# Performance work log

Hardware: AMD Instinct MI355X
Metric: run time of the kernel (lower is better)

The kernel has to match this reference:

```python
import jax, jax.numpy as jnp
import numpy as np

B, T, IN_DIM, D, H, NC = 4, 1024, 231, 512, 8, 1296
NL = 8          # 4 encoders x 2 layers each
DFF = 4 * D     # 2048
DH = D // H
EPS = 1e-5


def _p(k, shape, scale=0.02):
    return jax.random.normal(k, shape, jnp.float32) * scale


def setup_inputs() -> dict:
    key = jax.random.key(0)
    ks = iter(jax.random.split(key, 32))
    z = jnp.zeros
    o = jnp.ones
    return {
        'poses': jax.random.normal(next(ks), (B, T, IN_DIM), jnp.float32),
        'embed_w': _p(next(ks), (D, IN_DIM)), 'embed_b': z((D,)),
        'ln0_g': o((D,)), 'ln0_b': z((D,)),
        'inw': _p(next(ks), (NL, 3 * D, D)), 'inb': z((NL, 3 * D)),
        'outw': _p(next(ks), (NL, D, D)), 'outb': z((NL, D)),
        'ln1g': o((NL, D)), 'ln1b': z((NL, D)),
        'ln2g': o((NL, D)), 'ln2b': z((NL, D)),
        'ff1w': _p(next(ks), (NL, DFF, D)), 'ff1b': z((NL, DFF)),
        'ff2w': _p(next(ks), (NL, D, DFF)), 'ff2b': z((NL, D)),
        'conv1w': _p(next(ks), (D, D, 5)), 'conv1b': z((D,)),
        'bn1g': o((D,)), 'bn1b': z((D,)), 'bn1m': z((D,)), 'bn1v': o((D,)),
        'conv2w': _p(next(ks), (D, D, 3)), 'conv2b': z((D,)),
        'bn2g': o((D,)), 'bn2b': z((D,)), 'bn2m': z((D,)), 'bn2v': o((D,)),
        'fc1w': _p(next(ks), (D // 2, D)), 'fc1b': z((D // 2,)),
        'fc2w': _p(next(ks), (NC, D // 2)), 'fc2b': z((NC,)),
    }


def _ln(x, g, b):
    m = x.mean(-1, keepdims=True)
    v = x.var(-1, keepdims=True)
    return (x - m) / jnp.sqrt(v + EPS) * g + b


def _pos_enc(t_len, d, dtype):
    inv_freq = 1.0 / (10000.0 ** (jnp.arange(0, d, 2, dtype=jnp.float32) / d))
    sin_inp = jnp.arange(t_len, dtype=jnp.float32)[:, None] * inv_freq[None, :]  # [T, d/2]
    # interleave: even idx -> sin, odd idx -> cos
    return jnp.stack([jnp.sin(sin_inp), jnp.cos(sin_inp)], -1).reshape(t_len, d).astype(dtype)


def _layer(x, inw, inb, outw, outb, ln1g, ln1b, ln2g, ln2b, ff1w, ff1b, ff2w, ff2b):
    # pre-norm-style custom layer: norm1 before attention, residual add (no final norm)
    b_, t_, d_ = x.shape
    h = _ln(x, ln1g, ln1b)
    qkv = h @ inw.T + inb
    q, k, v = jnp.split(qkv, 3, axis=-1)
    heads = lambda z: z.reshape(b_, t_, H, DH).transpose(0, 2, 1, 3)  # [B,H,T,dh]
    q, k, v = heads(q), heads(k), heads(v)
    scores = jnp.einsum('bhqd,bhkd->bhqk', q, k) / np.float32(np.sqrt(DH))
    a = jax.nn.softmax(scores, axis=-1)  # explicit weights, as in torch need_weights=True path
    ctx = jnp.einsum('bhqk,bhkd->bhqd', a, v).transpose(0, 2, 1, 3).reshape(b_, t_, d_)
    x = x + ctx @ outw.T + outb
    h2 = _ln(x, ln2g, ln2b)
    ff = jax.nn.relu(h2 @ ff1w.T + ff1b) @ ff2w.T + ff2b
    return x + ff


def _bn(x, g, b, m, v):  # eval-mode BatchNorm1d over [B,C,T]
    return (x - m[None, :, None]) / jnp.sqrt(v + EPS)[None, :, None] * g[None, :, None] + b[None, :, None]


def _conv1d(x, w, b, pad):
    y = jax.lax.conv_general_dilated(x, w, (1,), ((pad, pad),),
                                     dimension_numbers=('NCH', 'OIH', 'NCH'))
    return y + b[None, :, None]


def reference(poses, embed_w, embed_b, ln0_g, ln0_b, inw, inb, outw, outb,
              ln1g, ln1b, ln2g, ln2b, ff1w, ff1b, ff2w, ff2b,
              conv1w, conv1b, bn1g, bn1b, bn1m, bn1v,
              conv2w, conv2b, bn2g, bn2b, bn2m, bn2v,
              fc1w, fc1b, fc2w, fc2b):
    x = _ln(poses @ embed_w.T + embed_b, ln0_g, ln0_b)
    x = x + _pos_enc(x.shape[1], D, x.dtype)[None]

    def block(y, idx):
        for i in idx:
            y = _layer(y, inw[i], inb[i], outw[i], outb[i], ln1g[i], ln1b[i],
                       ln2g[i], ln2b[i], ff1w[i], ff1b[i], ff2w[i], ff2b[i])
        return y

    x = block(x, (0, 1))
    x = block(x, (2, 3)) + x
    x = block(x, (4, 5)) + x
    x = block(x, (6, 7)) + x

    x = x.transpose(0, 2, 1)  # [B, D, T]
    tc = x.shape[-1]
    x = x.reshape(x.shape[0], x.shape[1], tc // 2, 2).mean(-1)  # AvgPool1d(2,2)
    x = jax.nn.gelu(_bn(_conv1d(x, conv1w, conv1b, 2), bn1g, bn1b, bn1m, bn1v), approximate=False)
    x = jax.nn.gelu(_bn(_conv1d(x, conv2w, conv2b, 1), bn2g, bn2b, bn2m, bn2v), approximate=False)
    x = x.transpose(0, 2, 1)  # [B, T/2, D]
    h = jax.nn.gelu(x @ fc1w.T + fc1b, approximate=False)
    return h @ fc2w.T + fc2b  # [B, T/2, num_classes]
```

## Files before the change

### kernel.cpp

```cpp
#include <hip/hip_runtime.h>
#include <math.h>

using u16 = unsigned short;
typedef __attribute__((ext_vector_type(8))) __bf16 bf16x8;
typedef __attribute__((ext_vector_type(4))) float f32x4;

constexpr int Bn = 4, Tn = 1024, INDIM = 231, Dm = 512, NCn = 1296;
constexpr int T2 = 512;
constexpr int Mseq = Bn * Tn;
constexpr int Mtc  = Bn * T2;

enum { EPI_BIAS = 0, EPI_BIAS_RELU, EPI_BIAS_RES, EPI_BIAS_GELU, EPI_SS_GELU };

__device__ __forceinline__ float gelu_exact(float x) {
    return 0.5f * x * (1.0f + erff(x * 0.70710678118654752f));
}
__device__ __forceinline__ u16 f2b(float f) {
    unsigned u = __builtin_bit_cast(unsigned, f);
    return (u16)((u + 0x7FFFu + ((u >> 16) & 1u)) >> 16);
}
__device__ __forceinline__ unsigned pack2(float a, float b) {
    return (unsigned)f2b(a) | ((unsigned)f2b(b) << 16);
}

typedef __attribute__((address_space(3))) void lds_void;
typedef __attribute__((address_space(1))) void g_void;
__device__ __forceinline__ void gld16(const void* g, void* l) {
    __builtin_amdgcn_global_load_lds((g_void*)(uintptr_t)g, (lds_void*)(uintptr_t)l, 16, 0, 0);
}

template<int EPI, bool OB, int IPAD, int OPAD, int MT>
__global__ __launch_bounds__(256)
void gemm_bf(const u16* __restrict__ A, int lda,
             const u16* __restrict__ W,
             float* __restrict__ Cf, u16* __restrict__ Cb,
             int M, int N, int K,
             const float* __restrict__ bias, const float* __restrict__ resid,
             const float* __restrict__ scale, const float* __restrict__ shift)
{
    constexpr int NR = (MT == 128) ? 4 : 2;
    constexpr int AI = MT / 32;
    __shared__ __align__(16) u16 As[2][MT * 64];
    __shared__ __align__(16) u16 Bs[2][128 * 64];
    const int tid = threadIdx.x;
    const int bm = blockIdx.y * MT, bn = blockIdx.x * 128;
    const int w = tid >> 6, lane = tid & 63;
    const int wr = (MT == 128) ? (w >> 1) * 64 : 0;
    const int wc = (MT == 128) ? (w & 1) * 64 : w * 32;
    const int lr = lane & 15, lhi = lane >> 4;

    const int srow = tid >> 3;
    const int cg8 = ((tid & 7) ^ (srow & 7)) * 8;
    const u16* apg[AI];
#pragma unroll
    for (int i = 0; i < AI; ++i) {
        const int r = bm + i * 32 + srow;
        apg[i] = A + (size_t)(r + 2 * IPAD * (r >> 9)) * lda + cg8;
    }
    const u16* wpg[4];
#pragma unroll
    for (int i = 0; i < 4; ++i) {
        int r = bn + i * 32 + srow; if (r >= N) r = N - 1;
        wpg[i] = W + (size_t)r * K + cg8;
    }

    f32x4 acc[4][NR] = {};
    const int nt = K >> 6;

#pragma unroll
    for (int i = 0; i < AI; ++i) gld16(apg[i], &As[0][(i * 256 + tid) * 8]);
#pragma unroll
    for (int i = 0; i < 4; ++i)  gld16(wpg[i], &Bs[0][(i * 256 + tid) * 8]);
    __syncthreads();

    for (int t = 0; t < nt; ++t) {
        const int cur = t & 1;
        if (t + 1 < nt) {
            const int k0 = (t + 1) * 64;
#pragma unroll
            for (int i = 0; i < AI; ++i) gld16(apg[i] + k0, &As[cur ^ 1][(i * 256 + tid) * 8]);
#pragma unroll
            for (int i = 0; i < 4; ++i)  gld16(wpg[i] + k0, &Bs[cur ^ 1][(i * 256 + tid) * 8]);
        }
#pragma unroll
        for (int ks = 0; ks < 2; ++ks) {
            bf16x8 af[4], bfv[NR];
#pragma unroll
            for (int m = 0; m < 4; ++m) {
                const int R = wr + lr + m * 16;
                af[m] = *(const bf16x8*)((const char*)&As[cur][0] + R * 128 + (((ks * 4 + lhi) ^ (R & 7)) * 16));
            }
#pragma unroll
            for (int n = 0; n < NR; ++n) {
                const int R = wc + lr + n * 16;
                bfv[n] = *(const bf16x8*)((const char*)&Bs[cur][0] + R * 128 + (((ks * 4 + lhi) ^ (R & 7)) * 16));
            }
#pragma unroll
            for (int m = 0; m < 4; ++m)
#pragma unroll
                for (int n = 0; n < NR; ++n)
                    acc[m][n] = __builtin_amdgcn_mfma_f32_16x16x32_bf16(af[m], bfv[n], acc[m][n], 0, 0, 0);
        }
        if (t + 1 < nt) __syncthreads();
    }

    const int col0 = bn + wc + lr;
    const int row0 = bm + wr + lhi * 4;
#pragma unroll
    for (int n = 0; n < NR; ++n) {
        const int col = col0 + n * 16;
        if (col >= N) continue;
        float bv = 0.f, sv = 0.f, hv = 0.f;
        if constexpr (EPI == EPI_SS_GELU) { sv = scale[col]; hv = shift[col]; }
        else bv = bias[col];
#pragma unroll
        for (int m = 0; m < 4; ++m) {
#pragma unroll
            for (int j = 0; j < 4; ++j) {
                const int r = row0 + m * 16 + j;
                const int orow = r + OPAD * (2 * (r >> 9) + 1);
                float o = acc[m][n][j];
                if constexpr (EPI == EPI_SS_GELU) {
                    o = gelu_exact(o * sv + hv);
                } else {
                    o += bv;
                    if constexpr (EPI == EPI_BIAS_RELU) o = fmaxf(o, 0.f);
                    if constexpr (EPI == EPI_BIAS_GELU) o = gelu_exact(o);
                    if constexpr (EPI == EPI_BIAS_RES) o += resid[(size_t)r * N + col];
                }
                if constexpr (OB) Cb[(size_t)orow * N + col] = f2b(o);
                else              Cf[(size_t)orow * N + col] = o;
            }
        }
    }
}

__global__ __launch_bounds__(256)
void attn_mfma(const u16* __restrict__ qkv, u16* __restrict__ out)
{
    const int b = blockIdx.z, h = blockIdx.y, q0 = blockIdx.x * 64;
    __shared__ __align__(16) u16 Ks[2][64 * 64];
    __shared__ __align__(16) u16 Vt[2][64 * 64];
    __shared__ __align__(16) float Ps[4][16 * 68];
    const int tid = threadIdx.x;
    const int w = tid >> 6, lane = tid & 63;
    const int lr = lane & 15, lhi = lane >> 4;
    const int kp = tid & 31, dc = (tid >> 5) * 8;
    const int krow = w * 8 + (lane >> 3);
    const int kcg = (((lane & 7) ^ (lane >> 3))) * 8;

    bf16x8 qf0, qf1;
    {
        const u16* qp = qkv + (size_t)(b * Tn + q0 + w * 16 + lr) * 1536 + h * 64 + lhi * 8;
        qf0 = *(const bf16x8*)qp;
        qf1 = *(const bf16x8*)(qp + 32);
    }
    float mrow[4], lrow[4];
#pragma unroll
    for (int j = 0; j < 4; ++j) { mrow[j] = -1e30f; lrow[j] = 0.f; }
    f32x4 oacc[4] = {};

    auto stageK = [&](int kb, int bsel) {
#pragma unroll
        for (int i = 0; i < 2; ++i)
            gld16(qkv + (size_t)(b * Tn + kb + i * 32 + krow) * 1536 + 512 + h * 64 + kcg,
                  &Ks[bsel][(i * 256 + tid) * 8]);
    };
    auto loadV = [&](int kb, uint4& rA, uint4& rB) {
        const u16* vp = qkv + (size_t)(b * Tn + kb + 2 * kp) * 1536 + 1024 + h * 64 + dc;
        rA = *(const uint4*)vp;
        rB = *(const uint4*)(vp + 1536);
    };
    auto vtrans = [&](uint4 rA, uint4 rB, int bsel) {
        const unsigned a0[4] = {rA.x, rA.y, rA.z, rA.w};
        const unsigned a1[4] = {rB.x, rB.y, rB.z, rB.w};
#pragma unroll
        for (int jj = 0; jj < 4; ++jj) {
            const int d0_ = dc + 2 * jj, d1_ = d0_ + 1;
            const unsigned w0 = (a0[jj] & 0xffffu) | (a1[jj] << 16);
            const unsigned w1 = (a0[jj] >> 16) | (a1[jj] & 0xffff0000u);
            *(unsigned*)((char*)&Vt[bsel][0] + d0_ * 128 + ((4 * kp) ^ ((d0_ & 7) << 4))) = w0;
            *(unsigned*)((char*)&Vt[bsel][0] + d1_ * 128 + ((4 * kp) ^ ((d1_ & 7) << 4))) = w1;
        }
    };

    uint4 vA, vB;
    stageK(0, 0);
    loadV(0, vA, vB);
    vtrans(vA, vB, 0);
    __syncthreads();

    constexpr float C1 = 0.125f * 1.44269504f;

    for (int kt = 0; kt < 16; ++kt) {
        const int cur = kt & 1;
        const bool more = kt < 15;
        if (more) {
            stageK((kt + 1) * 64, cur ^ 1);
            loadV((kt + 1) * 64, vA, vB);
        }
        __builtin_amdgcn_s_setprio(1);
        f32x4 s[4] = {};
#pragma unroll
        for (int t = 0; t < 4; ++t) {
            const int r = t * 16 + lr;
            const bf16x8 k0 = *(const bf16x8*)((const char*)&Ks[cur][0] + r * 128 + ((lhi * 16) ^ ((r & 7) << 4)));
            const bf16x8 k1 = *(const bf16x8*)((const char*)&Ks[cur][0] + r * 128 + ((64 + lhi * 16) ^ ((r & 7) << 4)));
            s[t] = __builtin_amdgcn_mfma_f32_16x16x32_bf16(qf0, k0, s[t], 0, 0, 0);
            s[t] = __builtin_amdgcn_mfma_f32_16x16x32_bf16(qf1, k1, s[t], 0, 0, 0);
        }
        __builtin_amdgcn_s_setprio(0);
        float f[4];
#pragma unroll
        for (int j = 0; j < 4; ++j) {
            float mt = fmaxf(fmaxf(s[0][j], s[1][j]), fmaxf(s[2][j], s[3][j]));
            mt = fmaxf(mt, __shfl_xor(mt, 1));
            mt = fmaxf(mt, __shfl_xor(mt, 2));
            mt = fmaxf(mt, __shfl_xor(mt, 4));
            mt = fmaxf(mt, __shfl_xor(mt, 8));
            const float mnew = fmaxf(mrow[j], mt);
            f[j] = exp2f((mrow[j] - mnew) * C1);
            mrow[j] = mnew;
            const float nb = mnew * C1;
            float sum = 0.f;
#pragma unroll
            for (int t = 0; t < 4; ++t) {
                const float p = exp2f(fmaf(s[t][j], C1, -nb));
                Ps[w][(lhi * 4 + j) * 68 + t * 16 + lr] = p;
                sum += p;
            }
            sum += __shfl_xor(sum, 1);
            sum += __shfl_xor(sum, 2);
            sum += __shfl_xor(sum, 4);
            sum += __shfl_xor(sum, 8);
            lrow[j] = lrow[j] * f[j] + sum;
        }
#pragma unroll
        for (int t = 0; t < 4; ++t)
#pragma unroll
            for (int j = 0; j < 4; ++j) oacc[t][j] *= f[j];
        asm volatile("s_waitcnt lgkmcnt(0)" ::: "memory");
        bf16x8 pf[2];
#pragma unroll
        for (int s2 = 0; s2 < 2; ++s2) {
            const float* pr = &Ps[w][lr * 68 + s2 * 32 + lhi * 8];
            const float4 pa = *(const float4*)pr;
            const float4 pb = *(const float4*)(pr + 4);
            uint4 pk;
            pk.x = pack2(pa.x, pa.y); pk.y = pack2(pa.z, pa.w);
            pk.z = pack2(pb.x, pb.y); pk.w = pack2(pb.z, pb.w);
            pf[s2] = __builtin_bit_cast(bf16x8, pk);
        }
        __builtin_amdgcn_s_setprio(1);
#pragma unroll
        for (int t = 0; t < 4; ++t) {
            const int rd = t * 16 + lr;
            const bf16x8 v0f = *(const bf16x8*)((const char*)&Vt[cur][0] + rd * 128 + ((lhi * 16) ^ ((rd & 7) << 4)));
            const bf16x8 v1f = *(const bf16x8*)((const char*)&Vt[cur][0] + rd * 128 + ((64 + lhi * 16) ^ ((rd & 7) << 4)));
            oacc[t] = __builtin_amdgcn_mfma_f32_16x16x32_bf16(pf[0], v0f, oacc[t], 0, 0, 0);
            oacc[t] = __builtin_amdgcn_mfma_f32_16x16x32_bf16(pf[1], v1f, oacc[t], 0, 0, 0);
        }
        __builtin_amdgcn_s_setprio(0);
        if (more) {
            vtrans(vA, vB, cur ^ 1);
            __syncthreads();
        }
    }
#pragma unroll
    for (int j = 0; j < 4; ++j) {
        const float inv = 1.f / lrow[j];
        const size_t grow = (size_t)(b * Tn + q0 + w * 16 + lhi * 4 + j) * 512 + h * 64;
#pragma unroll
        for (int t = 0; t < 4; ++t)
            out[grow + t * 16 + lr] = f2b(oacc[t][j] * inv);
    }
}

__device__ __forceinline__ float pe_val(int t, int d) {
    const int k = d & ~1;
    const float invf = __expf(-(float)k * (9.210340371976184f / 512.f));
    const float ang = (float)t * invf;
    return (d & 1) ? cosf(ang) : sinf(ang);
}

template<bool OB, bool PE>
__global__ __launch_bounds__(256)
void ln_k(const float* __restrict__ in, float* __restrict__ outf, u16* __restrict__ outb,
          const float* __restrict__ g, const float* __restrict__ bsh)
{
    const int lane = threadIdx.x & 63;
    const int row = blockIdx.x * 4 + (threadIdx.x >> 6);
    const float* src = in + (size_t)row * Dm;
    const int c0 = lane * 4;
    const float4 v0 = *(const float4*)(src + c0);
    const float4 v1 = *(const float4*)(src + 256 + c0);
    float s  = v0.x + v0.y + v0.z + v0.w + v1.x + v1.y + v1.z + v1.w;
    float ss = v0.x * v0.x + v0.y * v0.y + v0.z * v0.z + v0.w * v0.w
             + v1.x * v1.x + v1.y * v1.y + v1.z * v1.z + v1.w * v1.w;
#pragma unroll
    for (int off = 32; off; off >>= 1) { s += __shfl_xor(s, off); ss += __shfl_xor(ss, off); }
    const float mean = s * (1.f / 512.f);
    const float var = ss * (1.f / 512.f) - mean * mean;
    const float rstd = rsqrtf(var + 1e-5f);
    const float4 g0 = *(const float4*)(g + c0),   g1 = *(const float4*)(g + 256 + c0);
    const float4 b0 = *(const float4*)(bsh + c0), b1 = *(const float4*)(bsh + 256 + c0);
    float o0[4] = {(v0.x - mean) * rstd * g0.x + b0.x, (v0.y - mean) * rstd * g0.y + b0.y,
                   (v0.z - mean) * rstd * g0.z + b0.z, (v0.w - mean) * rstd * g0.w + b0.w};
    float o1[4] = {(v1.x - mean) * rstd * g1.x + b1.x, (v1.y - mean) * rstd * g1.y + b1.y,
                   (v1.z - mean) * rstd * g1.z + b1.z, (v1.w - mean) * rstd * g1.w + b1.w};
    if constexpr (PE) {
        const int t = row & (Tn - 1);
#pragma unroll
        for (int j = 0; j < 4; ++j) { o0[j] += pe_val(t, c0 + j); o1[j] += pe_val(t, 256 + c0 + j); }
    }
    if constexpr (OB) {
        *(ushort4*)(outb + (size_t)row * Dm + c0) =
            make_ushort4(f2b(o0[0]), f2b(o0[1]), f2b(o0[2]), f2b(o0[3]));
        *(ushort4*)(outb + (size_t)row * Dm + 256 + c0) =
            make_ushort4(f2b(o1[0]), f2b(o1[1]), f2b(o1[2]), f2b(o1[3]));
    } else {
        *(float4*)(outf + (size_t)row * Dm + c0) = make_float4(o0[0], o0[1], o0[2], o0[3]);
        *(float4*)(outf + (size_t)row * Dm + 256 + c0) = make_float4(o1[0], o1[1], o1[2], o1[3]);
    }
}

__global__ void copy_k(const float* __restrict__ a, float* __restrict__ o, int n4) {
    const int i = blockIdx.x * blockDim.x + threadIdx.x;
    if (i < n4) ((float4*)o)[i] = ((const float4*)a)[i];
}
__global__ void add_k(float* __restrict__ o, const float* __restrict__ a, int n4) {
    const int i = blockIdx.x * blockDim.x + threadIdx.x;
    if (i < n4) {
        float4 x = ((float4*)o)[i];
        const float4 y = ((const float4*)a)[i];
        x.x += y.x; x.y += y.y; x.z += y.z; x.w += y.w;
        ((float4*)o)[i] = x;
    }
}
__global__ void cvt_layer_k(const float* __restrict__ inw, const float* __restrict__ outw,
                            const float* __restrict__ ff1w, const float* __restrict__ ff2w,
                            int layer, u16* __restrict__ dst) {
    const int i = (blockIdx.x * 256 + threadIdx.x) * 8;
    const float* src;
    if (i < 786432)       src = inw  + (size_t)layer *  786432 + i;
    else if (i < 1048576) src = outw + (size_t)layer *  262144 + (i - 786432);
    else if (i < 2097152) src = ff1w + (size_t)layer * 1048576 + (i - 1048576);
    else                  src = ff2w + (size_t)layer * 1048576 + (i - 2097152);
    const float4 a = *(const float4*)src, b = *(const float4*)(src + 4);
    uint4 o; o.x = pack2(a.x, a.y); o.y = pack2(a.z, a.w); o.z = pack2(b.x, b.y); o.w = pack2(b.z, b.w);
    *(uint4*)(dst + i) = o;
}
__global__ void cvt8_k(const float* __restrict__ in, u16* __restrict__ out, int n8) {
    const int t = blockIdx.x * 256 + threadIdx.x;
    if (t >= n8) return;
    const int i = t * 8;
    const float4 a = *(const float4*)(in + i), b = *(const float4*)(in + i + 4);
    uint4 o; o.x = pack2(a.x, a.y); o.y = pack2(a.z, a.w); o.z = pack2(b.x, b.y); o.w = pack2(b.z, b.w);
    *(uint4*)(out + i) = o;
}
__global__ void padposes_k(const float* __restrict__ p, u16* __restrict__ o, int rows) {
    const int i = blockIdx.x * 256 + threadIdx.x;
    if (i >= rows * 256) return;
    const int r = i >> 8, c = i & 255;
    o[i] = (c < INDIM) ? f2b(p[r * INDIM + c]) : (u16)0;
}
__global__ void zero_k(uint4* __restrict__ p, int n16) {
    const int i = blockIdx.x * 256 + threadIdx.x;
    if (i < n16) p[i] = make_uint4(0, 0, 0, 0);
}
__global__ void pool_k(const float* __restrict__ x, u16* __restrict__ o) {
    const int i = blockIdx.x * 256 + threadIdx.x;
    if (i >= 262144) return;
    const int flat = i * 4;
    const int row = flat >> 9, col = flat & 511;
    const int b = row >> 9, t2 = row & 511;
    const float* p0 = x + ((size_t)(b * Tn + 2 * t2) << 9) + col;
    const float4 u = *(const float4*)p0;
    const float4 w = *(const float4*)(p0 + 512);
    ushort4 r = make_ushort4(f2b(0.5f * (u.x + w.x)), f2b(0.5f * (u.y + w.y)),
                             f2b(0.5f * (u.z + w.z)), f2b(0.5f * (u.w + w.w)));
    *(ushort4*)(o + (((size_t)(b * 516 + 2 + t2)) << 9) + col) = r;
}
__global__ void wtrans_k(const float* __restrict__ w, u16* __restrict__ wt, int KS) {
    const int i = blockIdx.x * 256 + threadIdx.x;
    if (i >= 512 * 512 * KS) return;
    const int o = i / (512 * KS);
    const int rem = i - o * (512 * KS);
    const int c = rem / KS, ks = rem - c * KS;
    wt[((size_t)o * KS + ks) * 512 + c] = f2b(w[i]);
}
__global__ void bnfold_k(const float* __restrict__ g, const float* __restrict__ b,
                         const float* __restrict__ m, const float* __restrict__ v,
                         const float* __restrict__ cb, float* __restrict__ sc, float* __restrict__ sh) {
    const int i = blockIdx.x * blockDim.x + threadIdx.x;
    if (i < Dm) {
        const float s = g[i] * rsqrtf(v[i] + 1e-5f);
        sc[i] = s;
        sh[i] = (cb[i] - m[i]) * s + b[i];
    }
}

extern "C" void kernel_launch(void* const* d_in, const int* in_sizes, int n_in,
                              void* d_out, int out_size, void* d_ws, size_t ws_size,
                              hipStream_t stream)
{
    (void)in_sizes; (void)n_in; (void)out_size; (void)ws_size;
    const float* poses   = (const float*)d_in[0];
    const float* embed_w = (const float*)d_in[1];
    const float* embed_b = (const float*)d_in[2];
    const float* ln0_g   = (const float*)d_in[3];
    const float* ln0_b   = (const float*)d_in[4];
    const float* inw  = (const float*)d_in[5];
    const float* inb  = (const float*)d_in[6];
    const float* outw = (const float*)d_in[7];
    const float* outb = (const float*)d_in[8];
    const float* ln1g = (const float*)d_in[9];
    const float* ln1b = (const float*)d_in[10];
    const float* ln2g = (const float*)d_in[11];
    const float* ln2b = (const float*)d_in[12];
    const float* ff1w = (const float*)d_in[13];
    const float* ff1b = (const float*)d_in[14];
    const float* ff2w = (const float*)d_in[15];
    const float* ff2b = (const float*)d_in[16];
    const float* conv1w = (const float*)d_in[17];
    const float* conv1b = (const float*)d_in[18];
    const float* bn1g = (const float*)d_in[19];
    const float* bn1b = (const float*)d_in[20];
    const float* bn1m = (const float*)d_in[21];
    const float* bn1v = (const float*)d_in[22];
    const float* conv2w = (const float*)d_in[23];
    const float* conv2b = (const float*)d_in[24];
    const float* bn2g = (const float*)d_in[25];
    const float* bn2b = (const float*)d_in[26];
    const float* bn2m = (const float*)d_in[27];
    const float* bn2v = (const float*)d_in[28];
    const float* fc1w = (const float*)d_in[29];
    const float* fc1b = (const float*)d_in[30];
    const float* fc2w = (const float*)d_in[31];
    const float* fc2b = (const float*)d_in[32];

    char* ws = (char*)d_ws;
    float* x    = (float*)(ws);
    float* resb = (float*)(ws + (8u << 20));
    char* big   = ws + (16u << 20);
    u16* qkv16  = (u16*)big;
    u16* hb16   = (u16*)(ws + (40u << 20));
    u16* ctx16  = (u16*)(ws + (44u << 20));
    u16* ff116  = (u16*)(ws + (48u << 20));
    u16* wbuf   = (u16*)(ws + (64u << 20));
    float* outp = (float*)d_out;

    char* tb = big;
    u16* poolpad = (u16*)tb;
    u16* c1pad   = (u16*)(tb + 2113536);
    u16* c2o16   = (u16*)(tb + 4218880);
    u16* f1o16   = (u16*)(tb + 6316032);
    u16* w1t16   = (u16*)(tb + 7364608);
    u16* w2t16   = (u16*)(tb + 9986048);
    u16* fc1w16  = (u16*)(tb + 11558912);
    u16* fc2w16  = (u16*)(tb + 11821056);
    float* sc1   = (float*)(tb + 12484608);
    float* sh1   = sc1 + 512;
    float* sc2   = sh1 + 512;
    float* sh2   = sc2 + 512;
    u16* embw16  = (u16*)(tb + (20u << 20));
    float* embout = (float*)(tb + (16u << 20));
    u16* pospad  = hb16;

    const u16* wq  = wbuf;
    const u16* wo  = wbuf + 786432;
    const u16* wf1 = wbuf + 1048576;
    const u16* wf2 = wbuf + 2097152;

    padposes_k<<<4096, 256, 0, stream>>>(poses, pospad, 4096);
    padposes_k<<<512, 256, 0, stream>>>(embed_w, embw16, 512);
    gemm_bf<EPI_BIAS, false, 0, 0, 64><<<dim3(4, 64), 256, 0, stream>>>(
        pospad, 256, embw16, embout, nullptr, Mseq, 512, 256, embed_b, nullptr, nullptr, nullptr);
    ln_k<false, true><<<1024, 256, 0, stream>>>(embout, x, nullptr, ln0_g, ln0_b);

    for (int i = 0; i < 8; ++i) {
        if (i == 2 || i == 4 || i == 6)
            copy_k<<<2048, 256, 0, stream>>>(x, resb, 1 << 19);
        cvt_layer_k<<<1536, 256, 0, stream>>>(inw, outw, ff1w, ff2w, i, wbuf);
        ln_k<true, false><<<1024, 256, 0, stream>>>(x, nullptr, hb16, ln1g + i * 512, ln1b + i * 512);
        gemm_bf<EPI_BIAS, true, 0, 0, 128><<<dim3(12, 32), 256, 0, stream>>>(
            hb16, 512, wq, nullptr, qkv16, Mseq, 1536, 512, inb + i * 1536, nullptr, nullptr, nullptr);
        attn_mfma<<<dim3(16, 8, 4), 256, 0, stream>>>(qkv16, ctx16);
        gemm_bf<EPI_BIAS_RES, false, 0, 0, 64><<<dim3(4, 64), 256, 0, stream>>>(
            ctx16, 512, wo, x, nullptr, Mseq, 512, 512, outb + i * 512, x, nullptr, nullptr);
        ln_k<true, false><<<1024, 256, 0, stream>>>(x, nullptr, hb16, ln2g + i * 512, ln2b + i * 512);
        gemm_bf<EPI_BIAS_RELU, true, 0, 0, 128><<<dim3(16, 32), 256, 0, stream>>>(
            hb16, 512, wf1, nullptr, ff116, Mseq, 2048, 512, ff1b + i * 2048, nullptr, nullptr, nullptr);
        gemm_bf<EPI_BIAS_RES, false, 0, 0, 64><<<dim3(4, 64), 256, 0, stream>>>(
            ff116, 2048, wf2, x, nullptr, Mseq, 512, 2048, ff2b + i * 512, x, nullptr, nullptr);
        if (i == 3 || i == 5 || i == 7)
            add_k<<<2048, 256, 0, stream>>>(x, resb, 1 << 19);
    }

    zero_k<<<516, 256, 0, stream>>>((uint4*)poolpad, 132096);
    pool_k<<<1024, 256, 0, stream>>>(x, poolpad);
    wtrans_k<<<5120, 256, 0, stream>>>(conv1w, w1t16, 5);
    bnfold_k<<<2, 256, 0, stream>>>(bn1g, bn1b, bn1m, bn1v, conv1b, sc1, sh1);
    zero_k<<<514, 256, 0, stream>>>((uint4*)c1pad, 131584);
    gemm_bf<EPI_SS_GELU, true, 2, 1, 64><<<dim3(4, 32), 256, 0, stream>>>(
        poolpad, 512, w1t16, nullptr, c1pad, Mtc, 512, 2560, nullptr, nullptr, sc1, sh1);
    wtrans_k<<<3072, 256, 0, stream>>>(conv2w, w2t16, 3);
    bnfold_k<<<2, 256, 0, stream>>>(bn2g, bn2b, bn2m, bn2v, conv2b, sc2, sh2);
    gemm_bf<EPI_SS_GELU, true, 1, 0, 64><<<dim3(4, 32), 256, 0, stream>>>(
        c1pad, 512, w2t16, nullptr, c2o16, Mtc, 512, 1536, nullptr, nullptr, sc2, sh2);
    cvt8_k<<<64, 256, 0, stream>>>(fc1w, fc1w16, 16384);
    cvt8_k<<<162, 256, 0, stream>>>(fc2w, fc2w16, 41472);
    gemm_bf<EPI_BIAS_GELU, true, 0, 0, 64><<<dim3(2, 32), 256, 0, stream>>>(
        c2o16, 512, fc1w16, nullptr, f1o16, Mtc, 256, 512, fc1b, nullptr, nullptr, nullptr);
    gemm_bf<EPI_BIAS, false, 0, 0, 64><<<dim3(11, 32), 256, 0, stream>>>(
        f1o16, 256, fc2w16, outp, nullptr, Mtc, 1296, 256, fc2b, nullptr, nullptr, nullptr);
}
```

Before: 1.304 ms.

## Fuse block residual adds into FF2 GEMM epilogue and keep attention P in registers

Measured after the change: 1.203 ms. 1.08x faster.

```diff
diff --git a/kernel.cpp b/kernel.cpp
--- a/kernel.cpp
+++ b/kernel.cpp
@@ -29,14 +29,15 @@
     __builtin_amdgcn_global_load_lds((g_void*)(uintptr_t)g, (lds_void*)(uintptr_t)l, 16, 0, 0);
 }
 
-template<int EPI, bool OB, int IPAD, int OPAD, int MT>
+template<int EPI, bool OB, int IPAD, int OPAD, int MT, int RM>
 __global__ __launch_bounds__(256)
 void gemm_bf(const u16* __restrict__ A, int lda,
              const u16* __restrict__ W,
              float* __restrict__ Cf, u16* __restrict__ Cb,
              int M, int N, int K,
              const float* __restrict__ bias, const float* __restrict__ resid,
-             const float* __restrict__ scale, const float* __restrict__ shift)
+             const float* __restrict__ scale, const float* __restrict__ shift,
+             const float* __restrict__ rb, float* __restrict__ rbw)
 {
     constexpr int NR = (MT == 128) ? 4 : 2;
     constexpr int AI = MT / 32;
@@ -126,8 +127,12 @@
                     o += bv;
                     if constexpr (EPI == EPI_BIAS_RELU) o = fmaxf(o, 0.f);
                     if constexpr (EPI == EPI_BIAS_GELU) o = gelu_exact(o);
-                    if constexpr (EPI == EPI_BIAS_RES) o += resid[(size_t)r * N + col];
+                    if constexpr (EPI == EPI_BIAS_RES) {
+                        o += resid[(size_t)r * N + col];
+                        if constexpr ((RM & 1) != 0) o += rb[(size_t)r * N + col];
+                    }
                 }
+                if constexpr ((RM & 2) != 0) rbw[(size_t)r * N + col] = o;
                 if constexpr (OB) Cb[(size_t)orow * N + col] = f2b(o);
                 else              Cf[(size_t)orow * N + col] = o;
             }
@@ -138,16 +143,18 @@
 __global__ __launch_bounds__(256)
 void attn_mfma(const u16* __restrict__ qkv, u16* __restrict__ out)
 {
-    const int b = blockIdx.z, h = blockIdx.y, q0 = blockIdx.x * 64;
+    const int bid = blockIdx.x;
+    const int qt = bid >> 5, g = bid & 31;
+    const int h = g & 7, b = g >> 3;
+    const int q0 = qt * 64;
     __shared__ __align__(16) u16 Ks[2][64 * 64];
     __shared__ __align__(16) u16 Vt[2][64 * 64];
-    __shared__ __align__(16) float Ps[4][16 * 68];
     const int tid = threadIdx.x;
     const int w = tid >> 6, lane = tid & 63;
     const int lr = lane & 15, lhi = lane >> 4;
     const int kp = tid & 31, dc = (tid >> 5) * 8;
-    const int krow = w * 8 + (lane >> 3);
-    const int kcg = (((lane & 7) ^ (lane >> 3))) * 8;
+    const int krow = tid >> 3;
+    const int kcg = ((lane & 7) ^ (lane >> 3)) * 8;
 
     bf16x8 qf0, qf1;
     {
@@ -155,9 +162,7 @@
         qf0 = *(const bf16x8*)qp;
         qf1 = *(const bf16x8*)(qp + 32);
     }
-    float mrow[4], lrow[4];
-#pragma unroll
-    for (int j = 0; j < 4; ++j) { mrow[j] = -1e30f; lrow[j] = 0.f; }
+    float mrow = -1e30f, lrow = 0.f;
     f32x4 oacc[4] = {};
 
     auto stageK = [&](int kb, int bsel) {
@@ -206,73 +211,79 @@
             const int r = t * 16 + lr;
             const bf16x8 k0 = *(const bf16x8*)((const char*)&Ks[cur][0] + r * 128 + ((lhi * 16) ^ ((r & 7) << 4)));
             const bf16x8 k1 = *(const bf16x8*)((const char*)&Ks[cur][0] + r * 128 + ((64 + lhi * 16) ^ ((r & 7) << 4)));
-            s[t] = __builtin_amdgcn_mfma_f32_16x16x32_bf16(qf0, k0, s[t], 0, 0, 0);
-            s[t] = __builtin_amdgcn_mfma_f32_16x16x32_bf16(qf1, k1, s[t], 0, 0, 0);
+            s[t] = __builtin_amdgcn_mfma_f32_16x16x32_bf16(k0, qf0, s[t], 0, 0, 0);
+            s[t] = __builtin_amdgcn_mfma_f32_16x16x32_bf16(k1, qf1, s[t], 0, 0, 0);
         }
         __builtin_amdgcn_s_setprio(0);
-        float f[4];
-#pragma unroll
-        for (int j = 0; j < 4; ++j) {
-            float mt = fmaxf(fmaxf(s[0][j], s[1][j]), fmaxf(s[2][j], s[3][j]));
-            mt = fmaxf(mt, __shfl_xor(mt, 1));
-            mt = fmaxf(mt, __shfl_xor(mt, 2));
-            mt = fmaxf(mt, __shfl_xor(mt, 4));
-            mt = fmaxf(mt, __shfl_xor(mt, 8));
-            const float mnew = fmaxf(mrow[j], mt);
-            f[j] = exp2f((mrow[j] - mnew) * C1);
-            mrow[j] = mnew;
-            const float nb = mnew * C1;
-            float sum = 0.f;
+        float mt = fmaxf(fmaxf(fmaxf(s[0][0], s[0][1]), fmaxf(s[0][2], s[0][3])),
+                         fmaxf(fmaxf(s[1][0], s[1][1]), fmaxf(s[1][2], s[1][3])));
+        mt = fmaxf(mt, fmaxf(fmaxf(fmaxf(s[2][0], s[2][1]), fmaxf(s[2][2], s[2][3])),
+                             fmaxf(fmaxf(s[3][0], s[3][1]), fmaxf(s[3][2], s[3][3]))));
+        mt = fmaxf(mt, __shfl_xor(mt, 16));
+        mt = fmaxf(mt, __shfl_xor(mt, 32));
+        const float mnew = fmaxf(mrow, mt);
+        const float f = exp2f((mrow - mnew) * C1);
+        mrow = mnew;
+        const float nb = mnew * C1;
+        float p[4][4];
+        float sum = 0.f;
+#pragma unroll
+        for (int t = 0; t < 4; ++t) {
+            float st = 0.f;
+#pragma unroll
+            for (int j = 0; j < 4; ++j) {
+                p[t][j] = exp2f(fmaf(s[t][j], C1, -nb));
+                st += p[t][j];
+            }
+            sum += st;
+        }
+        sum += __shfl_xor(sum, 16);
+        sum += __shfl_xor(sum, 32);
+        lrow = lrow * f + sum;
+#pragma unroll
+        for (int t = 0; t < 4; ++t)
+#pragma unroll
+            for (int j = 0; j < 4; ++j) oacc[t][j] *= f;
+        unsigned pw[4][2];
+#pragma unroll
+        for (int t = 0; t < 4; ++t) {
+            pw[t][0] = pack2(p[t][0], p[t][1]);
+            pw[t][1] = pack2(p[t][2], p[t][3]);
+        }
+        const int srcA = lr + ((lane & 16) << 1);
+        const int srcB = srcA + 16;
+        const bool hi2 = lane >= 32;
+#pragma unroll
+        for (int ks = 0; ks < 2; ++ks) {
+            const unsigned a0 = __shfl(pw[2 * ks][0], srcA), b0 = __shfl(pw[2 * ks + 1][0], srcA);
+            const unsigned a1 = __shfl(pw[2 * ks][1], srcA), b1 = __shfl(pw[2 * ks + 1][1], srcA);
+            const unsigned a2 = __shfl(pw[2 * ks][0], srcB), b2 = __shfl(pw[2 * ks + 1][0], srcB);
+            const unsigned a3 = __shfl(pw[2 * ks][1], srcB), b3 = __shfl(pw[2 * ks + 1][1], srcB);
+            uint4 bw;
+            bw.x = hi2 ? b0 : a0; bw.y = hi2 ? b1 : a1;
+            bw.z = hi2 ? b2 : a2; bw.w = hi2 ? b3 : a3;
+            const bf16x8 pf = __builtin_bit_cast(bf16x8, bw);
+            __builtin_amdgcn_s_setprio(1);
 #pragma unroll
             for (int t = 0; t < 4; ++t) {
-                const float p = exp2f(fmaf(s[t][j], C1, -nb));
-                Ps[w][(lhi * 4 + j) * 68 + t * 16 + lr] = p;
-                sum += p;
+                const int rd = t * 16 + lr;
+                const bf16x8 vf = *(const bf16x8*)((const char*)&Vt[cur][0] + rd * 128 + ((ks * 64 + lhi * 16) ^ ((rd & 7) << 4)));
+                oacc[t] = __builtin_amdgcn_mfma_f32_16x16x32_bf16(vf, pf, oacc[t], 0, 0, 0);
             }
-            sum += __shfl_xor(sum, 1);
-            sum += __shfl_xor(sum, 2);
-            sum += __shfl_xor(sum, 4);
-            sum += __shfl_xor(sum, 8);
-            lrow[j] = lrow[j] * f[j] + sum;
-        }
-#pragma unroll
-        for (int t = 0; t < 4; ++t)
-#pragma unroll
-            for (int j = 0; j < 4; ++j) oacc[t][j] *= f[j];
-        asm volatile("s_waitcnt lgkmcnt(0)" ::: "memory");
-        bf16x8 pf[2];
-#pragma unroll
-        for (int s2 = 0; s2 < 2; ++s2) {
-            const float* pr = &Ps[w][lr * 68 + s2 * 32 + lhi * 8];
-            const float4 pa = *(const float4*)pr;
-            const float4 pb = *(const float4*)(pr + 4);
-            uint4 pk;
-            pk.x = pack2(pa.x, pa.y); pk.y = pack2(pa.z, pa.w);
-            pk.z = pack2(pb.x, pb.y); pk.w = pack2(pb.z, pb.w);
-            pf[s2] = __builtin_bit_cast(bf16x8, pk);
-        }
-        __builtin_amdgcn_s_setprio(1);
-#pragma unroll
-        for (int t = 0; t < 4; ++t) {
-            const int rd = t * 16 + lr;
-            const bf16x8 v0f = *(const bf16x8*)((const char*)&Vt[cur][0] + rd * 128 + ((lhi * 16) ^ ((rd & 7) << 4)));
-            const bf16x8 v1f = *(const bf16x8*)((const char*)&Vt[cur][0] + rd * 128 + ((64 + lhi * 16) ^ ((rd & 7) << 4)));
-            oacc[t] = __builtin_amdgcn_mfma_f32_16x16x32_bf16(pf[0], v0f, oacc[t], 0, 0, 0);
-            oacc[t] = __builtin_amdgcn_mfma_f32_16x16x32_bf16(pf[1], v1f, oacc[t], 0, 0, 0);
-        }
-        __builtin_amdgcn_s_setprio(0);
+            __builtin_amdgcn_s_setprio(0);
+        }
         if (more) {
             vtrans(vA, vB, cur ^ 1);
             __syncthreads();
         }
     }
-#pragma unroll
-    for (int j = 0; j < 4; ++j) {
-        const float inv = 1.f / lrow[j];
-        const size_t grow = (size_t)(b * Tn + q0 + w * 16 + lhi * 4 + j) * 512 + h * 64;
-#pragma unroll
-        for (int t = 0; t < 4; ++t)
-            out[grow + t * 16 + lr] = f2b(oacc[t][j] * inv);
+    const float inv = 1.f / lrow;
+    const size_t base = (size_t)(b * Tn + q0 + w * 16 + lr) * 512 + h * 64;
+#pragma unroll
+    for (int t = 0; t < 4; ++t) {
+        ushort4 st = make_ushort4(f2b(oacc[t][0] * inv), f2b(oacc[t][1] * inv),
+                                  f2b(oacc[t][2] * inv), f2b(oacc[t][3] * inv));
+        *(ushort4*)&out[base + t * 16 + lhi * 4] = st;
     }
 }
 
@@ -324,19 +335,6 @@
     }
 }
 
-__global__ void copy_k(const float* __restrict__ a, float* __restrict__ o, int n4) {
-    const int i = blockIdx.x * blockDim.x + threadIdx.x;
-    if (i < n4) ((float4*)o)[i] = ((const float4*)a)[i];
-}
-__global__ void add_k(float* __restrict__ o, const float* __restrict__ a, int n4) {
-    const int i = blockIdx.x * blockDim.x + threadIdx.x;
-    if (i < n4) {
-        float4 x = ((float4*)o)[i];
-        const float4 y = ((const float4*)a)[i];
-        x.x += y.x; x.y += y.y; x.z += y.z; x.w += y.w;
-        ((float4*)o)[i] = x;
-    }
-}
 __global__ void cvt_layer_k(const float* __restrict__ inw, const float* __restrict__ outw,
                             const float* __restrict__ ff1w, const float* __restrict__ ff2w,
                             int layer, u16* __restrict__ dst) {
@@ -474,27 +472,33 @@
 
     padposes_k<<<4096, 256, 0, stream>>>(poses, pospad, 4096);
     padposes_k<<<512, 256, 0, stream>>>(embed_w, embw16, 512);
-    gemm_bf<EPI_BIAS, false, 0, 0, 64><<<dim3(4, 64), 256, 0, stream>>>(
-        pospad, 256, embw16, embout, nullptr, Mseq, 512, 256, embed_b, nullptr, nullptr, nullptr);
+    gemm_bf<EPI_BIAS, false, 0, 0, 64, 0><<<dim3(4, 64), 256, 0, stream>>>(
+        pospad, 256, embw16, embout, nullptr, Mseq, 512, 256, embed_b, nullptr, nullptr, nullptr, nullptr, nullptr);
     ln_k<false, true><<<1024, 256, 0, stream>>>(embout, x, nullptr, ln0_g, ln0_b);
 
     for (int i = 0; i < 8; ++i) {
-        if (i == 2 || i == 4 || i == 6)
-            copy_k<<<2048, 256, 0, stream>>>(x, resb, 1 << 19);
         cvt_layer_k<<<1536, 256, 0, stream>>>(inw, outw, ff1w, ff2w, i, wbuf);
         ln_k<true, false><<<1024, 256, 0, stream>>>(x, nullptr, hb16, ln1g + i * 512, ln1b + i * 512);
-        gemm_bf<EPI_BIAS, true, 0, 0, 128><<<dim3(12, 32), 256, 0, stream>>>(
-            hb16, 512, wq, nullptr, qkv16, Mseq, 1536, 512, inb + i * 1536, nullptr, nullptr, nullptr);
-        attn_mfma<<<dim3(16, 8, 4), 256, 0, stream>>>(qkv16, ctx16);
-        gemm_bf<EPI_BIAS_RES, false, 0, 0, 64><<<dim3(4, 64), 256, 0, stream>>>(
-            ctx16, 512, wo, x, nullptr, Mseq, 512, 512, outb + i * 512, x, nullptr, nullptr);
+        gemm_bf<EPI_BIAS, true, 0, 0, 128, 0><<<dim3(12, 32), 256, 0, stream>>>(
+            hb16, 512, wq, nullptr, qkv16, Mseq, 1536, 512, inb + i * 1536, nullptr, nullptr, nullptr, nullptr, nullptr);
+        attn_mfma<<<dim3(512), 256, 0, stream>>>(qkv16, ctx16);
+        gemm_bf<EPI_BIAS_RES, false, 0, 0, 64, 0><<<dim3(4, 64), 256, 0, stream>>>(
+            ctx16, 512, wo, x, nullptr, Mseq, 512, 512, outb + i * 512, x, nullptr, nullptr, nullptr, nullptr);
         ln_k<true, false><<<1024, 256, 0, stream>>>(x, nullptr, hb16, ln2g + i * 512, ln2b + i * 512);
-        gemm_bf<EPI_BIAS_RELU, true, 0, 0, 128><<<dim3(16, 32), 256, 0, stream>>>(
-            hb16, 512, wf1, nullptr, ff116, Mseq, 2048, 512, ff1b + i * 2048, nullptr, nullptr, nullptr);
-        gemm_bf<EPI_BIAS_RES, false, 0, 0, 64><<<dim3(4, 64), 256, 0, stream>>>(
-            ff116, 2048, wf2, x, nullptr, Mseq, 512, 2048, ff2b + i * 512, x, nullptr, nullptr);
-        if (i == 3 || i == 5 || i == 7)
-            add_k<<<2048, 256, 0, stream>>>(x, resb, 1 << 19);
+        gemm_bf<EPI_BIAS_RELU, true, 0, 0, 128, 0><<<dim3(16, 32), 256, 0, stream>>>(
+            hb16, 512, wf1, nullptr, ff116, Mseq, 2048, 512, ff1b + i * 2048, nullptr, nullptr, nullptr, nullptr, nullptr);
+        if (i == 1)
+            gemm_bf<EPI_BIAS_RES, false, 0, 0, 64, 2><<<dim3(4, 64), 256, 0, stream>>>(
+                ff116, 2048, wf2, x, nullptr, Mseq, 512, 2048, ff2b + i * 512, x, nullptr, nullptr, nullptr, resb);
+        else if (i == 3 || i == 5)
+            gemm_bf<EPI_BIAS_RES, false, 0, 0, 64, 3><<<dim3(4, 64), 256, 0, stream>>>(
+                ff116, 2048, wf2, x, nullptr, Mseq, 512, 2048, ff2b + i * 512, x, nullptr, nullptr, resb, resb);
+        else if (i == 7)
+            gemm_bf<EPI_BIAS_RES, false, 0, 0, 64, 1><<<dim3(4, 64), 256, 0, stream>>>(
+                ff116, 2048, wf2, x, nullptr, Mseq, 512, 2048, ff2b + i * 512, x, nullptr, nullptr, resb, nullptr);
+        else
+            gemm_bf<EPI_BIAS_RES, false, 0, 0, 64, 0><<<dim3(4, 64), 256, 0, stream>>>(
+                ff116, 2048, wf2, x, nullptr, Mseq, 512, 2048, ff2b + i * 512, x, nullptr, nullptr, nullptr, nullptr);
     }
 
     zero_k<<<516, 256, 0, stream>>>((uint4*)poolpad, 132096);
@@ -502,16 +506,16 @@
     wtrans_k<<<5120, 256, 0, stream>>>(conv1w, w1t16, 5);
     bnfold_k<<<2, 256, 0, stream>>>(bn1g, bn1b, bn1m, bn1v, conv1b, sc1, sh1);
     zero_k<<<514, 256, 0, stream>>>((uint4*)c1pad, 131584);
-    gemm_bf<EPI_SS_GELU, true, 2, 1, 64><<<dim3(4, 32), 256, 0, stream>>>(
-        poolpad, 512, w1t16, nullptr, c1pad, Mtc, 512, 2560, nullptr, nullptr, sc1, sh1);
+    gemm_bf<EPI_SS_GELU, true, 2, 1, 64, 0><<<dim3(4, 32), 256, 0, stream>>>(
+        poolpad, 512, w1t16, nullptr, c1pad, Mtc, 512, 2560, nullptr, nullptr, sc1, sh1, nullptr, nullptr);
     wtrans_k<<<3072, 256, 0, stream>>>(conv2w, w2t16, 3);
     bnfold_k<<<2, 256, 0, stream>>>(bn2g, bn2b, bn2m, bn2v, conv2b, sc2, sh2);
-    gemm_bf<EPI_SS_GELU, true, 1, 0, 64><<<dim3(4, 32), 256, 0, stream>>>(
-        c1pad, 512, w2t16, nullptr, c2o16, Mtc, 512, 1536, nullptr, nullptr, sc2, sh2);
+    gemm_bf<EPI_SS_GELU, true, 1, 0, 64, 0><<<dim3(4, 32), 256, 0, stream>>>(
+        c1pad, 512, w2t16, nullptr, c2o16, Mtc, 512, 1536, nullptr, nullptr, sc2, sh2, nullptr, nullptr);
     cvt8_k<<<64, 256, 0, stream>>>(fc1w, fc1w16, 16384);
     cvt8_k<<<162, 256, 0, stream>>>(fc2w, fc2w16, 41472);
-    gemm_bf<EPI_BIAS_GELU, true, 0, 0, 64><<<dim3(2, 32), 256, 0, stream>>>(
-        c2o16, 512, fc1w16, nullptr, f1o16, Mtc, 256, 512, fc1b, nullptr, nullptr, nullptr);
-    gemm_bf<EPI_BIAS, false, 0, 0, 64><<<dim3(11, 32), 256, 0, stream>>>(
-        f1o16, 256, fc2w16, outp, nullptr, Mtc, 1296, 256, fc2b, nullptr, nullptr, nullptr);
-}
+    gemm_bf<EPI_BIAS_GELU, true, 0, 0, 64, 0><<<dim3(2, 32), 256, 0, stream>>>(
+        c2o16, 512, fc1w16, nullptr, f1o16, Mtc, 256, 512, fc1b, nullptr, nullptr, nullptr, nullptr, nullptr);
+    gemm_bf<EPI_BIAS, false, 0, 0, 64, 0><<<dim3(11, 32), 256, 0, stream>>>(
+        f1o16, 256, fc2w16, outp, nullptr, Mtc, 1296, 256, fc2b, nullptr, nullptr, nullptr, nullptr, nullptr);
+}
```
